# Kernel tuning notes

Measured on AMD Instinct MI355X. Metric: run time of the kernel, lower is better.

Reference implementation:

```python
import jax, jax.numpy as jnp
import numpy as np

B, S, D = 1, 2048, 1024
H, DH = 16, 64
FF_INNER = 4 * D          # 4096
FUSED = 2 * FF_INNER      # 8192
ROT_BASE = 1000.0


def _rope_tables(seq_len, dim_head):
    # rotarizer: inv_freq = (base ** (arange(0, dh, 2)/dh)) ** -1 ; cached in bfloat16
    inv_freq = 1.0 / (ROT_BASE ** (jnp.arange(0, dim_head, 2, dtype=jnp.float32) / dim_head))
    t = jnp.arange(seq_len, dtype=jnp.float32)
    freqs = jnp.outer(t, inv_freq)                     # [S, DH/2]
    cos = jnp.cos(freqs).astype(jnp.bfloat16)[None, :, None, :]  # [1,S,1,DH/2]
    sin = jnp.sin(freqs).astype(jnp.bfloat16)[None, :, None, :]
    return cos, sin


def _apply_rope(x, cos, sin):
    d = x.shape[-1] // 2
    x1, x2 = x[..., :d], x[..., d:]
    y1 = x1 * cos + x2 * sin
    y2 = -x1 * sin + x2 * cos
    return jnp.concatenate([y1, y2], axis=-1).astype(x.dtype)


def _l2norm(x):
    # F.normalize(p=2, dim=-1), eps=1e-12
    n = jnp.linalg.norm(x, axis=-1, keepdims=True)
    return x / jnp.maximum(n, 1e-12)


def setup_inputs() -> dict:
    key = jax.random.key(0)
    ks = jax.random.split(key, 12)
    std = 0.02
    inp = {
        "h_states": jax.random.normal(ks[0], (B, S, D), jnp.float32),
        "Wq": jax.random.normal(ks[1], (D, D), jnp.float32) * std,
        "Wk": jax.random.normal(ks[2], (D, D), jnp.float32) * std,
        "Wv": jax.random.normal(ks[3], (D, D), jnp.float32) * std,
        "Wqb": jax.random.normal(ks[4], (D, D), jnp.float32) * std,
        "Wkb": jax.random.normal(ks[5], (D, D), jnp.float32) * std,
        "Wo": jax.random.normal(ks[6], (D, D), jnp.float32) * std,
        "bo": jnp.zeros((D,), jnp.float32),
        "W1": jax.random.normal(ks[7], (D, FUSED), jnp.float32) * std,
        "b1": jnp.zeros((FUSED,), jnp.float32),
        "W2": jax.random.normal(ks[8], (FF_INNER, D), jnp.float32) * std,
        "b2": jnp.zeros((D,), jnp.float32),
        "learnedlambda": jnp.asarray(1.0, jnp.float32),
        # l2normscale init: log(S^2 - S) for training_seqlen S
        "l2normscale": jnp.asarray(np.log(float(S) ** 2 - float(S)), np.float32),
    }
    return inp


def reference(h_states, Wq, Wk, Wv, Wqb, Wkb, Wo, bo, W1, b1, W2, b2, learnedlambda, l2normscale):
    b, s, d = h_states.shape
    scale = DH ** -0.5

    # layerwisenorm: RMSNorm, no affine
    eps = jnp.finfo(h_states.dtype).eps
    x = h_states * jax.lax.rsqrt(jnp.mean(jnp.square(h_states), axis=-1, keepdims=True) + eps)

    # projections -> [B,S,H,DH]
    def proj(W):
        return (x @ W).reshape(b, s, H, DH)
    q, k, v = proj(Wq), proj(Wk), proj(Wv)
    qb, kb = proj(Wqb), proj(Wkb)

    cos, sin = _rope_tables(s, DH)
    # per-head qk-norm (l2norm) then rope; v untouched
    q = _apply_rope(_l2norm(q), cos, sin)
    k = _apply_rope(_l2norm(k), cos, sin)
    qb = _apply_rope(_l2norm(qb), cos, sin)
    kb = _apply_rope(_l2norm(kb), cos, sin)

    causal = jnp.tril(jnp.ones((s, s), bool))  # [S,S]

    # main attention: scale=1 (l2norm path), causal softmax, scaled by l2normscale
    scores = jnp.einsum("bqhd,bkhd->bhqk", q, k)
    scores = jnp.where(causal[None, None], scores, -jnp.inf)
    attn = jax.nn.softmax(scores, axis=-1)
    y = l2normscale * jnp.einsum("bhqk,bkhd->bhqd", attn, v)  # [B,H,S,DH]

    # bias attention: masked raw scores @ ones == causal row-sum, broadcast over DH
    sb = jnp.einsum("bqhd,bkhd->bhqk", qb, kb) * scale
    sb = jnp.where(causal[None, None], sb, 0.0)
    y = y + jnp.sum(sb, axis=-1, keepdims=True)  # broadcast over head dim

    y = y.transpose(0, 2, 1, 3).reshape(b, s, d)
    attn_out = y @ Wo + bo

    # fused SwiGLU: chunk -> (x_part, gate); silu(gate) * x_part
    u = x @ W1 + b1
    xp, gate = u[..., :FF_INNER], u[..., FF_INNER:]
    ff = (jax.nn.silu(gate) * xp) @ W2 + b2

    return h_states * learnedlambda + ff + attn_out
```

## Files before the change

### kernel.cpp

```cpp
#include <hip/hip_runtime.h>
#include <hip/hip_bf16.h>
#include <math.h>

typedef __bf16 bf16x8 __attribute__((ext_vector_type(8)));
typedef float  f32x4  __attribute__((ext_vector_type(4)));

#define GLD16(g, l) __builtin_amdgcn_global_load_lds(                      \
    (const __attribute__((address_space(1))) void*)(g),                    \
    (__attribute__((address_space(3))) void*)(l), 16, 0, 0)

#define SCHED_FENCE() __builtin_amdgcn_sched_barrier(0)


__device__ __forceinline__ void tconv_tile(const float* __restrict__ in,
                                           __bf16* __restrict__ out,
                                           int ldin, int ldout,
                                           int r0, int c0, int tid) {
  __shared__ float t[32][33];
  int tx = tid & 31, ty = tid >> 5;
  #pragma unroll
  for (int i = ty; i < 32; i += 8)
    t[i][tx] = in[(size_t)(r0 + i) * ldin + c0 + tx];
  __syncthreads();
  #pragma unroll
  for (int i = ty; i < 32; i += 8)
    out[(size_t)(c0 + i) * ldout + r0 + tx] = (__bf16)t[tx][i];
}

__global__ __launch_bounds__(256) void tconv_k(const float* __restrict__ in,
                                               __bf16* __restrict__ out,
                                               int ldin, int ldout) {
  tconv_tile(in, out, ldin, ldout, blockIdx.y * 32, blockIdx.x * 32, threadIdx.x);
}

__global__ __launch_bounds__(256) void tconvw1p_k(const float* __restrict__ W1,
                                                  __bf16* __restrict__ out) {
  int c0 = blockIdx.x * 32;
  int src_c0 = ((c0 >> 5) & 1) * 4096 + (c0 >> 6) * 32;
  __shared__ float t[32][33];
  int r0 = blockIdx.y * 32;
  int tid = threadIdx.x, tx = tid & 31, ty = tid >> 5;
  #pragma unroll
  for (int i = ty; i < 32; i += 8)
    t[i][tx] = W1[(size_t)(r0 + i) * 8192 + src_c0 + tx];
  __syncthreads();
  #pragma unroll
  for (int i = ty; i < 32; i += 8)
    out[(size_t)(c0 + i) * 1024 + r0 + tx] = (__bf16)t[tx][i];
}

__global__ __launch_bounds__(256) void tconv5_k(const float* __restrict__ w0,
    const float* __restrict__ w1, const float* __restrict__ w2,
    const float* __restrict__ w3, const float* __restrict__ w4,
    __bf16* __restrict__ out) {
  const float* src[5] = {w0, w1, w2, w3, w4};
  int z = blockIdx.z;
  tconv_tile(src[z], out + (size_t)z * 1048576, 1024, 1024,
             blockIdx.y * 32, blockIdx.x * 32, threadIdx.x);
}

__global__ __launch_bounds__(256) void tconvwow2_k(const float* __restrict__ Wo,
    const float* __restrict__ W2, __bf16* __restrict__ WoW2t) {
  int tid = threadIdx.x;
  if (blockIdx.z == 0) {
    if (blockIdx.y >= 32) return;
    __shared__ float t[32][33];
    int r0 = blockIdx.y * 32, c0 = blockIdx.x * 32;
    int tx = tid & 31, ty = tid >> 5;
    #pragma unroll
    for (int i = ty; i < 32; i += 8)
      t[i][tx] = Wo[(size_t)(r0 + i) * 1024 + c0 + tx];
    __syncthreads();
    #pragma unroll
    for (int i = ty; i < 32; i += 8)
      WoW2t[(size_t)(c0 + i) * 5120 + r0 + tx] = (__bf16)t[tx][i];
  } else {
    __shared__ float t[32][33];
    int r0 = blockIdx.y * 32, c0 = blockIdx.x * 32;
    int tx = tid & 31, ty = tid >> 5;
    #pragma unroll
    for (int i = ty; i < 32; i += 8)
      t[i][tx] = W2[(size_t)(r0 + i) * 1024 + c0 + tx];
    __syncthreads();
    #pragma unroll
    for (int i = ty; i < 32; i += 8)
      WoW2t[(size_t)(c0 + i) * 5120 + 1024 + r0 + tx] = (__bf16)t[tx][i];
  }
}

__global__ __launch_bounds__(256) void rmsnorm_k(const float* __restrict__ hs,
                                                 __bf16* __restrict__ x) {
  int row = blockIdx.x, tid = threadIdx.x;
  const float4 v = ((const float4*)(hs + (size_t)row * 1024))[tid];
  float ss = v.x * v.x + v.y * v.y + v.z * v.z + v.w * v.w;
  #pragma unroll
  for (int o = 32; o > 0; o >>= 1) ss += __shfl_xor(ss, o);
  __shared__ float ps[4];
  if ((tid & 63) == 0) ps[tid >> 6] = ss;
  __syncthreads();
  float tot = ps[0] + ps[1] + ps[2] + ps[3];
  float r = rsqrtf(tot * (1.0f / 1024.0f) + 1.1920929e-7f);
  __bf16* xr = x + (size_t)row * 1024 + tid * 4;
  xr[0] = (__bf16)(v.x * r); xr[1] = (__bf16)(v.y * r);
  xr[2] = (__bf16)(v.z * r); xr[3] = (__bf16)(v.w * r);
}

__global__ __launch_bounds__(256, 3) void gemm_bt_k(
    const __bf16* __restrict__ A, const __bf16* __restrict__ Bt,
    float* __restrict__ C, int N, int K) {
  __shared__ __bf16 sA[3][128 * 32];
  __shared__ __bf16 sB[3][128 * 32];
  const int tid = threadIdx.x;
  const int lane = tid & 63;
  const int quad = lane >> 4, l16 = lane & 15;
  const int wave = tid >> 6;
  const int waveM = wave >> 1, waveN = wave & 1;
  const int m0 = blockIdx.y * 128, n0 = blockIdx.x * 128;
  const int nk = K >> 5;
  const int rowS = tid >> 2;
  const int kg = ((tid & 3) ^ ((rowS >> 1) & 3)) * 8;
  const __bf16* gA0 = A + (size_t)(m0 + rowS) * K + kg;
  const __bf16* gA1 = gA0 + (size_t)64 * K;
  const __bf16* gB0 = Bt + (size_t)(n0 + rowS) * K + kg;
  const __bf16* gB1 = gB0 + (size_t)64 * K;
  const int lo0 = tid * 8, lo1 = 2048 + tid * 8;

  auto stage = [&](int t) {
    int s = t % 3;
    __bf16* dA = sA[s];
    __bf16* dB = sB[s];
    GLD16(gA0 + t * 32, dA + lo0);
    GLD16(gA1 + t * 32, dA + lo1);
    GLD16(gB0 + t * 32, dB + lo0);
    GLD16(gB1 + t * 32, dB + lo1);
  };
  stage(0); stage(1);

  f32x4 acc[4][4] = {};
  #pragma unroll 1
  for (int i = 0; i < nk; ++i) {
    if (i < nk - 1)
      asm volatile("s_waitcnt vmcnt(4)" ::: "memory");
    else
      asm volatile("s_waitcnt vmcnt(0)" ::: "memory");
    __builtin_amdgcn_s_barrier();
    SCHED_FENCE();
    int cs = i % 3;
    const __bf16* cA = sA[cs];
    const __bf16* cB = sB[cs];
    if (i + 2 < nk) stage(i + 2);
    SCHED_FENCE();
    bf16x8 af[4], bfv[4];
    #pragma unroll
    for (int mt = 0; mt < 4; ++mt) {
      int r = waveM * 64 + mt * 16 + l16;
      af[mt] = *(const bf16x8*)(cA + r * 32 + ((quad ^ ((r >> 1) & 3)) * 8));
    }
    #pragma unroll
    for (int nt = 0; nt < 4; ++nt) {
      int r = waveN * 64 + nt * 16 + l16;
      bfv[nt] = *(const bf16x8*)(cB + r * 32 + ((quad ^ ((r >> 1) & 3)) * 8));
    }
    __builtin_amdgcn_s_setprio(1);
    #pragma unroll
    for (int mt = 0; mt < 4; ++mt)
      #pragma unroll
      for (int nt = 0; nt < 4; ++nt)
        acc[mt][nt] = __builtin_amdgcn_mfma_f32_16x16x32_bf16(af[mt], bfv[nt], acc[mt][nt], 0, 0, 0);
    __builtin_amdgcn_s_setprio(0);
    SCHED_FENCE();
  }
  #pragma unroll
  for (int mt = 0; mt < 4; ++mt) {
    int row = m0 + waveM * 64 + mt * 16 + quad * 4;
    #pragma unroll
    for (int nt = 0; nt < 4; ++nt) {
      int col = n0 + waveN * 64 + nt * 16 + l16;
      #pragma unroll
      for (int r = 0; r < 4; ++r)
        C[(size_t)(row + r) * N + col] = acc[mt][nt][r];
    }
  }
}

__global__ __launch_bounds__(256, 3) void gemm_partk_k(
    const __bf16* __restrict__ A, const __bf16* __restrict__ Bt,
    float* __restrict__ P, int N, int K) {
  __shared__ __bf16 sA[3][128 * 32];
  __shared__ __bf16 sB[3][128 * 32];
  const int tid = threadIdx.x;
  const int lane = tid & 63;
  const int quad = lane >> 4, l16 = lane & 15;
  const int wave = tid >> 6;
  const int waveM = wave >> 1, waveN = wave & 1;
  const int m0 = blockIdx.y * 128, n0 = blockIdx.x * 128;
  const int kz = blockIdx.z, nz = gridDim.z;
  const int kper = K / nz, kbeg = kz * kper;
  const int nk = kper >> 5;
  const size_t MN = (size_t)gridDim.y * 128 * N;
  float* C = P + (size_t)kz * MN;
  const int rowS = tid >> 2;
  const int kg = ((tid & 3) ^ ((rowS >> 1) & 3)) * 8;
  const __bf16* gA0 = A + (size_t)(m0 + rowS) * K + kbeg + kg;
  const __bf16* gA1 = gA0 + (size_t)64 * K;
  const __bf16* gB0 = Bt + (size_t)(n0 + rowS) * K + kbeg + kg;
  const __bf16* gB1 = gB0 + (size_t)64 * K;
  const int lo0 = tid * 8, lo1 = 2048 + tid * 8;

  auto stage = [&](int t) {
    int s = t % 3;
    __bf16* dA = sA[s];
    __bf16* dB = sB[s];
    GLD16(gA0 + t * 32, dA + lo0);
    GLD16(gA1 + t * 32, dA + lo1);
    GLD16(gB0 + t * 32, dB + lo0);
    GLD16(gB1 + t * 32, dB + lo1);
  };
  stage(0); stage(1);

  f32x4 acc[4][4] = {};
  #pragma unroll 1
  for (int i = 0; i < nk; ++i) {
    if (i < nk - 1)
      asm volatile("s_waitcnt vmcnt(4)" ::: "memory");
    else
      asm volatile("s_waitcnt vmcnt(0)" ::: "memory");
    __builtin_amdgcn_s_barrier();
    SCHED_FENCE();
    int cs = i % 3;
    const __bf16* cA = sA[cs];
    const __bf16* cB = sB[cs];
    if (i + 2 < nk) stage(i + 2);
    SCHED_FENCE();
    bf16x8 af[4], bfv[4];
    #pragma unroll
    for (int mt = 0; mt < 4; ++mt) {
      int r = waveM * 64 + mt * 16 + l16;
      af[mt] = *(const bf16x8*)(cA + r * 32 + ((quad ^ ((r >> 1) & 3)) * 8));
    }
    #pragma unroll
    for (int nt = 0; nt < 4; ++nt) {
      int r = waveN * 64 + nt * 16 + l16;
      bfv[nt] = *(const bf16x8*)(cB + r * 32 + ((quad ^ ((r >> 1) & 3)) * 8));
    }
    __builtin_amdgcn_s_setprio(1);
    #pragma unroll
    for (int mt = 0; mt < 4; ++mt)
      #pragma unroll
      for (int nt = 0; nt < 4; ++nt)
        acc[mt][nt] = __builtin_amdgcn_mfma_f32_16x16x32_bf16(af[mt], bfv[nt], acc[mt][nt], 0, 0, 0);
    __builtin_amdgcn_s_setprio(0);
    SCHED_FENCE();
  }
  #pragma unroll
  for (int mt = 0; mt < 4; ++mt) {
    int row = m0 + waveM * 64 + mt * 16 + quad * 4;
    #pragma unroll
    for (int nt = 0; nt < 4; ++nt) {
      int col = n0 + waveN * 64 + nt * 16 + l16;
      #pragma unroll
      for (int r = 0; r < 4; ++r)
        C[(size_t)(row + r) * N + col] = acc[mt][nt][r];
    }
  }
}

__global__ __launch_bounds__(512, 2) void ffn1silu_k(
    const __bf16* __restrict__ A, const __bf16* __restrict__ W1t,
    const float* __restrict__ b1, __bf16* __restrict__ ffout) {
  __shared__ __bf16 sA[4][256 * 32];
  __shared__ __bf16 sB[4][256 * 32];
  const int tid = threadIdx.x, lane = tid & 63, w = tid >> 6;
  const int quad = lane >> 4, l16 = lane & 15;
  const int wm = w >> 2, wn = w & 3;
  const int m0 = blockIdx.y * 256;
  const int n0p = blockIdx.x * 256;
  const int K = 1024, NKT = 32;
  const int rowS = tid >> 2;
  const int kg = ((tid & 3) ^ ((rowS >> 1) & 3)) * 8;
  const __bf16* gA0 = A + (size_t)(m0 + rowS) * K + kg;
  const __bf16* gA1 = gA0 + (size_t)128 * K;
  const __bf16* gB0 = W1t + (size_t)(n0p + rowS) * K + kg;
  const __bf16* gB1 = gB0 + (size_t)128 * K;
  const int lo0 = tid * 8, lo1 = 4096 + tid * 8;

  f32x4 acc[8][4] = {};

  auto stageA = [&](int t) {
    __bf16* d = sA[t & 3];
    GLD16(gA0 + t * 32, d + lo0);
    GLD16(gA1 + t * 32, d + lo1);
  };
  auto stageB = [&](int t) {
    __bf16* d = sB[t & 3];
    GLD16(gB0 + t * 32, d + lo0);
    GLD16(gB1 + t * 32, d + lo1);
  };

  auto compute_half = [&](const __bf16* cA, const bf16x8* bfr, int half) {
    bf16x8 af[4];
    #pragma unroll
    for (int mt = 0; mt < 4; ++mt) {
      int r = wm * 128 + half * 64 + mt * 16 + l16;
      af[mt] = *(const bf16x8*)(cA + r * 32 + ((quad ^ ((r >> 1) & 3)) * 8));
    }
    __builtin_amdgcn_s_setprio(1);
    #pragma unroll
    for (int mt = 0; mt < 4; ++mt)
      #pragma unroll
      for (int nt = 0; nt < 4; ++nt)
        acc[half * 4 + mt][nt] = __builtin_amdgcn_mfma_f32_16x16x32_bf16(
            af[mt], bfr[nt], acc[half * 4 + mt][nt], 0, 0, 0);
    __builtin_amdgcn_s_setprio(0);
  };

  stageA(0); stageB(0);
  stageA(1); stageB(1);
  stageA(2); stageB(2);

  #pragma unroll 1
  for (int t = 0; t < NKT; ++t) {
    if (t < NKT - 2)
      asm volatile("s_waitcnt vmcnt(8)" ::: "memory");
    else if (t == NKT - 2)
      asm volatile("s_waitcnt vmcnt(4)" ::: "memory");
    else
      asm volatile("s_waitcnt vmcnt(0)" ::: "memory");
    __builtin_amdgcn_s_barrier();
    SCHED_FENCE();
    const __bf16* cA = sA[t & 3];
    const __bf16* cB = sB[t & 3];
    if (t + 3 < NKT) stageA(t + 3);
    SCHED_FENCE();
    bf16x8 bfr[4];
    #pragma unroll
    for (int nt = 0; nt < 4; ++nt) {
      int r = wn * 64 + nt * 16 + l16;
      bfr[nt] = *(const bf16x8*)(cB + r * 32 + ((quad ^ ((r >> 1) & 3)) * 8));
    }
    compute_half(cA, bfr, 0);
    SCHED_FENCE();
    if (t + 3 < NKT) stageB(t + 3);
    SCHED_FENCE();
    compute_half(cA, bfr, 1);
    SCHED_FENCE();
  }

  const int colbase = (blockIdx.x * 4 + wn) * 32;
  #pragma unroll
  for (int j = 0; j < 8; ++j) {
    int row = m0 + wm * 128 + (j >> 2) * 64 + (j & 3) * 16 + quad * 4;
    #pragma unroll
    for (int p = 0; p < 2; ++p) {
      int col = colbase + p * 16 + l16;
      float bxv = b1[col], bgv = b1[col + 4096];
      #pragma unroll
      for (int r = 0; r < 4; ++r) {
        float xp = acc[j][p][r] + bxv;
        float g  = acc[j][p + 2][r] + bgv;
        float val = xp * g / (1.f + __expf(-g));
        ffout[(size_t)(row + r) * 5120 + 1024 + col] = (__bf16)val;
      }
    }
  }
}

__global__ __launch_bounds__(256) void combine_k(
    const float* __restrict__ P, const float* __restrict__ b2,
    const float* __restrict__ bo, const float* __restrict__ hs,
    const float* __restrict__ plam, float* __restrict__ out) {
  const size_t MN = (size_t)2048 * 1024;
  size_t i = ((size_t)blockIdx.x * 256 + threadIdx.x) * 4;
  int col = (int)(i & 1023);
  float4 a0 = *(const float4*)(P + i);
  float4 a1 = *(const float4*)(P + MN + i);
  float4 a2 = *(const float4*)(P + 2 * MN + i);
  float4 a3 = *(const float4*)(P + 3 * MN + i);
  float4 h  = *(const float4*)(hs + i);
  float4 v2 = *(const float4*)(b2 + col);
  float4 vo = *(const float4*)(bo + col);
  float lam = plam[0];
  float4 o;
  o.x = (a0.x + a1.x) + (a2.x + a3.x) + v2.x + vo.x + lam * h.x;
  o.y = (a0.y + a1.y) + (a2.y + a3.y) + v2.y + vo.y + lam * h.y;
  o.z = (a0.z + a1.z) + (a2.z + a3.z) + v2.z + vo.z + lam * h.z;
  o.w = (a0.w + a1.w) + (a2.w + a3.w) + v2.w + vo.w + lam * h.w;
  *(float4*)(out + i) = o;
}

__global__ __launch_bounds__(256) void qkprep_k(const float* __restrict__ proj,
    __bf16* __restrict__ qo, __bf16* __restrict__ ko,
    float* __restrict__ qbo, float* __restrict__ kbo) {
  int gw = blockIdx.x * 4 + (threadIdx.x >> 6);
  int lane = threadIdx.x & 63;
  int s = gw >> 4, h = gw & 15;
  int j = lane & 31;
  float inv = exp2f(-0.31143076f * (float)j);
  float ang = (float)s * inv;
  float cb = (float)(__bf16)__cosf(ang);
  float sb = (float)(__bf16)__sinf(ang);
  size_t ibase = (size_t)s * 5120 + h * 64 + lane;
  size_t obase = (size_t)s * 1024 + h * 64 + lane;
  bool lo = lane < 32;

  auto proc = [&](const float* src) -> float {
    float xv = src[ibase];
    float ss = xv * xv;
    #pragma unroll
    for (int o = 32; o > 0; o >>= 1) ss += __shfl_xor(ss, o);
    float y = xv / fmaxf(sqrtf(ss), 1e-12f);
    float yp = __shfl_xor(y, 32);
    return lo ? (y * cb + yp * sb) : (y * cb - yp * sb);
  };
  qo[obase]  = (__bf16)proc(proj + 0);
  ko[obase]  = (__bf16)proc(proj + 1024);
  qbo[obase] = proc(proj + 3072);
  kbo[obase] = proc(proj + 4096);
}

__global__ __launch_bounds__(256) void kbsum_k(const float* __restrict__ kb,
                                               float* __restrict__ tsum,
                                               float* __restrict__ tsum8) {
  int t = blockIdx.x, h = blockIdx.y;
  int d = threadIdx.x & 63, w = threadIdx.x >> 6;
  size_t base = (size_t)h * 64 + d;
  float s = 0.f;
  #pragma unroll
  for (int r = 0; r < 8; ++r)
    s += kb[(size_t)(t * 32 + w * 8 + r) * 1024 + base];
  tsum8[(size_t)((t * 4 + w) * 16 + h) * 64 + d] = s;
  __shared__ float ps[4][64];
  ps[w][d] = s;
  __syncthreads();
  if (w == 0)
    tsum[(size_t)(t * 16 + h) * 64 + d] = (ps[0][d] + ps[1][d]) + (ps[2][d] + ps[3][d]);
}

__global__ __launch_bounds__(256) void sbrow2_k(const float* __restrict__ qb,
                                                const float* __restrict__ kb,
                                                const float* __restrict__ tsum,
                                                const float* __restrict__ tsum8,
                                                float* __restrict__ sb) {
  int t = blockIdx.x, h = blockIdx.y;
  int d = threadIdx.x & 63, g = threadIdx.x >> 6;
  size_t base = (size_t)h * 64 + d;
  float run = 0.f;
  for (int tp = 0; tp < t; ++tp) run += tsum[(size_t)(tp * 16 + h) * 64 + d];
  for (int w = 0; w < g; ++w) run += tsum8[(size_t)((t * 4 + w) * 16 + h) * 64 + d];
  int r0 = t * 32 + g * 8;
  for (int s0 = 0; s0 < 8; s0 += 4) {
    float p[4];
    #pragma unroll
    for (int u = 0; u < 4; ++u) {
      size_t off = (size_t)(r0 + s0 + u) * 1024 + base;
      run += kb[off];
      p[u] = qb[off] * run;
    }
    #pragma unroll
    for (int o = 32; o > 0; o >>= 1) {
      #pragma unroll
      for (int u = 0; u < 4; ++u) p[u] += __shfl_xor(p[u], o);
    }
    if (d == 0) {
      #pragma unroll
      for (int u = 0; u < 4; ++u) sb[(r0 + s0 + u) * 16 + h] = 0.125f * p[u];
    }
  }
}

__global__ __launch_bounds__(256) void attn_k(const __bf16* __restrict__ qg,
    const __bf16* __restrict__ kg, const __bf16* __restrict__ vtg,
    float* __restrict__ o_part, float* __restrict__ m_part,
    float* __restrict__ l_part) {
  __shared__ __bf16 sK[2][64 * 64];
  __shared__ __bf16 sVt[2][64 * 64];
  __shared__ __bf16 sP[4][16 * 64];
  const int pair = blockIdx.x, j4 = blockIdx.y, hh = blockIdx.z;
  const int tid = threadIdx.x, lane = tid & 63, w = tid >> 6;
  const int quad = lane >> 4, l16 = lane & 15;
  const int srow = tid >> 3;
  const int sg = (tid & 7) ^ (srow & 7);
  __bf16* sPw = sP[w];

  auto stage = [&](int kt) {
    int b = kt & 1;
    const __bf16* gK = kg + (size_t)(kt * 64 + srow) * 1024 + hh * 64 + sg * 8;
    const __bf16* gV = vtg + (size_t)(hh * 64 + srow) * 2048 + kt * 64 + sg * 8;
    GLD16(gK, sK[b] + tid * 8);
    GLD16(gK + (size_t)32 * 1024, sK[b] + tid * 8 + 2048);
    GLD16(gV, sVt[b] + tid * 8);
    GLD16(gV + (size_t)32 * 2048, sVt[b] + tid * 8 + 2048);
  };

  for (int phase = 0; phase < 2; ++phase) {
    const int qt = phase ? 31 - pair : pair;
    const int q0 = qt * 64;
    const int n = qt + 1;
    const int kb = (j4 * n) >> 2, ke = ((j4 + 1) * n) >> 2;
    bf16x8 qf[2];
    #pragma unroll
    for (int kk = 0; kk < 2; ++kk)
      qf[kk] = *(const bf16x8*)(qg + (size_t)(q0 + w * 16 + l16) * 1024 + hh * 64 + kk * 32 + quad * 8);
    f32x4 accO[4] = {};
    float m_[4], l_[4];
    #pragma unroll
    for (int r = 0; r < 4; ++r) { m_[r] = -INFINITY; l_[r] = 0.f; }

    __syncthreads();
    if (kb < ke) stage(kb);

    for (int kt = kb; kt < ke; ++kt) {
      __syncthreads();
      SCHED_FENCE();
      if (kt + 1 < ke) stage(kt + 1);
      SCHED_FENCE();
      const __bf16* cK = sK[kt & 1];
      const __bf16* cV = sVt[kt & 1];

      f32x4 s4[4];
      #pragma unroll
      for (int nt = 0; nt < 4; ++nt) {
        int r = nt * 16 + l16;
        bf16x8 b0 = *(const bf16x8*)(cK + r * 64 + ((quad ^ (r & 7)) * 8));
        bf16x8 b1 = *(const bf16x8*)(cK + r * 64 + (((4 + quad) ^ (r & 7)) * 8));
        f32x4 sa = {0.f, 0.f, 0.f, 0.f};
        sa = __builtin_amdgcn_mfma_f32_16x16x32_bf16(qf[0], b0, sa, 0, 0, 0);
        sa = __builtin_amdgcn_mfma_f32_16x16x32_bf16(qf[1], b1, sa, 0, 0, 0);
        s4[nt] = sa;
      }
      if (kt == qt) {
        #pragma unroll
        for (int nt = 0; nt < 4; ++nt)
          #pragma unroll
          for (int r = 0; r < 4; ++r)
            if (nt * 16 + l16 > w * 16 + quad * 4 + r) s4[nt][r] = -INFINITY;
      }
      float mx[4], al[4], rs[4];
      #pragma unroll
      for (int r = 0; r < 4; ++r)
        mx[r] = fmaxf(fmaxf(s4[0][r], s4[1][r]), fmaxf(s4[2][r], s4[3][r]));
      #pragma unroll
      for (int o = 1; o < 16; o <<= 1)
        #pragma unroll
        for (int r = 0; r < 4; ++r) mx[r] = fmaxf(mx[r], __shfl_xor(mx[r], o));
      #pragma unroll
      for (int r = 0; r < 4; ++r) {
        float mn = fmaxf(m_[r], mx[r]);
        al[r] = __expf(m_[r] - mn);
        m_[r] = mn;
      }
      float p[4][4];
      #pragma unroll
      for (int nt = 0; nt < 4; ++nt)
        #pragma unroll
        for (int r = 0; r < 4; ++r)
          p[nt][r] = __expf(s4[nt][r] - m_[r]);
      #pragma unroll
      for (int r = 0; r < 4; ++r)
        rs[r] = (p[0][r] + p[1][r]) + (p[2][r] + p[3][r]);
      #pragma unroll
      for (int o = 1; o < 16; o <<= 1)
        #pragma unroll
        for (int r = 0; r < 4; ++r) rs[r] += __shfl_xor(rs[r], o);
      #pragma unroll
      for (int r = 0; r < 4; ++r) l_[r] = l_[r] * al[r] + rs[r];
      #pragma unroll
      for (int nt = 0; nt < 4; ++nt)
        #pragma unroll
        for (int r = 0; r < 4; ++r) accO[nt][r] *= al[r];
      #pragma unroll
      for (int nt = 0; nt < 4; ++nt)
        #pragma unroll
        for (int r = 0; r < 4; ++r) {
          int row = quad * 4 + r, col = nt * 16 + l16;
          sPw[row * 64 + (col ^ ((row & 7) << 3))] = (__bf16)p[nt][r];
        }
      #pragma unroll
      for (int kk = 0; kk < 2; ++kk) {
        bf16x8 a = *(const bf16x8*)(sPw + l16 * 64 + (((kk * 4 + quad) ^ (l16 & 7)) * 8));
        #pragma unroll
        for (int nt = 0; nt < 4; ++nt) {
          int vr = nt * 16 + l16;
          bf16x8 bv = *(const bf16x8*)(cV + vr * 64 + (((kk * 4 + quad) ^ (vr & 7)) * 8));
          accO[nt] = __builtin_amdgcn_mfma_f32_16x16x32_bf16(a, bv, accO[nt], 0, 0, 0);
        }
      }
    }
    #pragma unroll
    for (int r = 0; r < 4; ++r) {
      int grow = q0 + w * 16 + quad * 4 + r;
      if (l16 == 0) {
        m_part[((size_t)j4 * 2048 + grow) * 16 + hh] = m_[r];
        l_part[((size_t)j4 * 2048 + grow) * 16 + hh] = l_[r];
      }
      #pragma unroll
      for (int nt = 0; nt < 4; ++nt)
        o_part[((size_t)j4 * 2048 + grow) * 1024 + hh * 64 + nt * 16 + l16] = accO[nt][r];
    }
  }
}

__global__ __launch_bounds__(256) void attnmerge_k(const float* __restrict__ o_part,
    const float* __restrict__ m_part, const float* __restrict__ l_part,
    const float* __restrict__ sbr, const float* __restrict__ pl2s,
    __bf16* __restrict__ yo) {
  int idx = blockIdx.x * 256 + threadIdx.x;
  int s = idx >> 8, rem = idx & 255;
  int h = rem >> 4, dg = (rem & 15) * 4;
  float m[4], l[4];
  #pragma unroll
  for (int j = 0; j < 4; ++j) {
    m[j] = m_part[((size_t)j * 2048 + s) * 16 + h];
    l[j] = l_part[((size_t)j * 2048 + s) * 16 + h];
  }
  float M = fmaxf(fmaxf(m[0], m[1]), fmaxf(m[2], m[3]));
  float den = 0.f;
  float4 acc = {0.f, 0.f, 0.f, 0.f};
  #pragma unroll
  for (int j = 0; j < 4; ++j) {
    float e = __expf(m[j] - M);
    den += l[j] * e;
    float4 o = *(const float4*)(o_part + ((size_t)j * 2048 + s) * 1024 + h * 64 + dg);
    acc.x += e * o.x; acc.y += e * o.y; acc.z += e * o.z; acc.w += e * o.w;
  }
  float sc = pl2s[0] / den;
  float add = sbr[s * 16 + h];
  __bf16* yp = yo + (size_t)s * 5120 + h * 64 + dg;
  yp[0] = (__bf16)(sc * acc.x + add);
  yp[1] = (__bf16)(sc * acc.y + add);
  yp[2] = (__bf16)(sc * acc.z + add);
  yp[3] = (__bf16)(sc * acc.w + add);
}

extern "C" void kernel_launch(void* const* d_in, const int* in_sizes, int n_in,
                              void* d_out, int out_size, void* d_ws, size_t ws_size,
                              hipStream_t stream) {
  (void)in_sizes; (void)n_in; (void)out_size; (void)ws_size;
  const float* hs   = (const float*)d_in[0];
  const float* Wq   = (const float*)d_in[1];
  const float* Wk   = (const float*)d_in[2];
  const float* Wv   = (const float*)d_in[3];
  const float* Wqb  = (const float*)d_in[4];
  const float* Wkb  = (const float*)d_in[5];
  const float* Wo   = (const float*)d_in[6];
  const float* bo   = (const float*)d_in[7];
  const float* W1   = (const float*)d_in[8];
  const float* b1   = (const float*)d_in[9];
  const float* W2   = (const float*)d_in[10];
  const float* b2   = (const float*)d_in[11];
  const float* plam = (const float*)d_in[12];
  const float* pl2s = (const float*)d_in[13];
  float* out = (float*)d_out;
  char* ws = (char*)d_ws;

  size_t off = 0;
  auto alloc = [&](size_t bytes) { char* p = ws + off; off += (bytes + 255) & ~(size_t)255; return p; };
  __bf16* Wt5    = (__bf16*)alloc((size_t)5 * 1024 * 1024 * 2);
  __bf16* WoW2t  = (__bf16*)alloc((size_t)1024 * 5120 * 2);
  __bf16* W1t    = (__bf16*)alloc((size_t)8192 * 1024 * 2);
  __bf16* xbf    = (__bf16*)alloc((size_t)2048 * 1024 * 2);
  __bf16* concat = (__bf16*)alloc((size_t)2048 * 5120 * 2);
  float*  proj  = (float*)alloc((size_t)2048 * 5120 * 4);
  float*  qbf32 = (float*)alloc((size_t)2048 * 1024 * 4);
  float*  kbf32 = (float*)alloc((size_t)2048 * 1024 * 4);
  __bf16* qbf   = (__bf16*)alloc((size_t)2048 * 1024 * 2);
  __bf16* kbf   = (__bf16*)alloc((size_t)2048 * 1024 * 2);
  float*  o_part = proj;
  float*  m_part = qbf32;
  float*  l_part = qbf32 + (size_t)4 * 2048 * 16;
  float*  gpart  = proj;
  __bf16* vtbf  = (__bf16*)alloc((size_t)1024 * 2048 * 2);
  float*  sbrow = (float*)alloc((size_t)2048 * 16 * 4);
  float*  tsum  = (float*)alloc((size_t)64 * 16 * 64 * 4);
  float*  tsum8 = (float*)alloc((size_t)256 * 16 * 64 * 4);

  tconv5_k<<<dim3(32, 32, 5), 256, 0, stream>>>(Wq, Wk, Wv, Wqb, Wkb, Wt5);
  tconvwow2_k<<<dim3(32, 128, 2), 256, 0, stream>>>(Wo, W2, WoW2t);
  tconvw1p_k<<<dim3(256, 32), 256, 0, stream>>>(W1, W1t);

  rmsnorm_k<<<2048, 256, 0, stream>>>(hs, xbf);
  gemm_bt_k<<<dim3(40, 16), 256, 0, stream>>>(xbf, Wt5, proj, 5120, 1024);
  qkprep_k<<<8192, 256, 0, stream>>>(proj, qbf, kbf, qbf32, kbf32);
  tconv_k<<<dim3(32, 64), 256, 0, stream>>>(proj + 2048, vtbf, 5120, 2048);
  kbsum_k<<<dim3(64, 16), 256, 0, stream>>>(kbf32, tsum, tsum8);
  sbrow2_k<<<dim3(64, 16), 256, 0, stream>>>(qbf32, kbf32, tsum, tsum8, sbrow);
  attn_k<<<dim3(16, 4, 16), 256, 0, stream>>>(qbf, kbf, vtbf, o_part, m_part, l_part);
  attnmerge_k<<<2048, 256, 0, stream>>>(o_part, m_part, l_part, sbrow, pl2s, concat);
  ffn1silu_k<<<dim3(32, 8), 512, 0, stream>>>(xbf, W1t, b1, concat);
  gemm_partk_k<<<dim3(8, 16, 4), 256, 0, stream>>>(concat, WoW2t, gpart, 1024, 5120);
  combine_k<<<2048, 256, 0, stream>>>(gpart, b2, bo, hs, plam, out);
}
```

Measured before the change: 361.2 us.

## Fuse qk l2norm+RoPE into QKV GEMM epilogue and merge weight repack launches

Moves the per-head L2 normalization and rotary embedding into the QKV projection GEMM's epilogue. Each wave's 64-column tile is exactly one head, so the norm is a 16-lane shuffle reduction, and q/k/qb/kb are written directly in their final formats. V is written to a compact buffer. This removes the separate qkprep kernel and the write and read-back of the full fp32 projection. The three weight transpose/convert kernels are also merged into one flat-grid repack kernel to cut launch overhead. The cost is extra epilogue math and more registers in the GEMM.

```diff
diff --git a/kernel.cpp b/kernel.cpp
--- a/kernel.cpp
+++ b/kernel.cpp
@@ -12,12 +12,56 @@
 #define SCHED_FENCE() __builtin_amdgcn_sched_barrier(0)
 
 
-__device__ __forceinline__ void tconv_tile(const float* __restrict__ in,
-                                           __bf16* __restrict__ out,
-                                           int ldin, int ldout,
-                                           int r0, int c0, int tid) {
+__global__ __launch_bounds__(256) void repack_k(
+    const float* __restrict__ Wq, const float* __restrict__ Wk,
+    const float* __restrict__ Wv, const float* __restrict__ Wqb,
+    const float* __restrict__ Wkb, const float* __restrict__ Wo,
+    const float* __restrict__ W2, const float* __restrict__ W1,
+    __bf16* __restrict__ Wt5, __bf16* __restrict__ WoW2t,
+    __bf16* __restrict__ W1t) {
+  int t = blockIdx.x;
+  const float* in; __bf16* outp;
+  int ldin, ldout, r0, c0, cin0, oofs;
+  if (t < 5120) {
+    int w = t >> 10, rem = t & 1023;
+    const float* src[5] = {Wq, Wk, Wv, Wqb, Wkb};
+    in = src[w]; ldin = 1024;
+    r0 = (rem >> 5) << 5; c0 = (rem & 31) << 5; cin0 = c0;
+    outp = Wt5 + (size_t)w * 1048576; ldout = 1024; oofs = 0;
+  } else if (t < 6144) {
+    int rem = t - 5120;
+    in = Wo; ldin = 1024;
+    r0 = (rem >> 5) << 5; c0 = (rem & 31) << 5; cin0 = c0;
+    outp = WoW2t; ldout = 5120; oofs = 0;
+  } else if (t < 10240) {
+    int rem = t - 6144;
+    in = W2; ldin = 1024;
+    r0 = (rem >> 5) << 5; c0 = (rem & 31) << 5; cin0 = c0;
+    outp = WoW2t; ldout = 5120; oofs = 1024;
+  } else {
+    int rem = t - 10240;
+    in = W1; ldin = 8192;
+    c0 = (rem & 255) << 5; r0 = (rem >> 8) << 5;
+    cin0 = ((c0 >> 5) & 1) * 4096 + (c0 >> 6) * 32;
+    outp = W1t; ldout = 1024; oofs = 0;
+  }
+  __shared__ float sh[32][33];
+  int tid = threadIdx.x, tx = tid & 31, ty = tid >> 5;
+  #pragma unroll
+  for (int i = ty; i < 32; i += 8)
+    sh[i][tx] = in[(size_t)(r0 + i) * ldin + cin0 + tx];
+  __syncthreads();
+  #pragma unroll
+  for (int i = ty; i < 32; i += 8)
+    outp[(size_t)(c0 + i) * ldout + oofs + r0 + tx] = (__bf16)sh[tx][i];
+}
+
+__global__ __launch_bounds__(256) void tconv_k(const float* __restrict__ in,
+                                               __bf16* __restrict__ out,
+                                               int ldin, int ldout) {
   __shared__ float t[32][33];
-  int tx = tid & 31, ty = tid >> 5;
+  int r0 = blockIdx.y * 32, c0 = blockIdx.x * 32;
+  int tid = threadIdx.x, tx = tid & 31, ty = tid >> 5;
   #pragma unroll
   for (int i = ty; i < 32; i += 8)
     t[i][tx] = in[(size_t)(r0 + i) * ldin + c0 + tx];
@@ -25,67 +69,6 @@
   #pragma unroll
   for (int i = ty; i < 32; i += 8)
     out[(size_t)(c0 + i) * ldout + r0 + tx] = (__bf16)t[tx][i];
-}
-
-__global__ __launch_bounds__(256) void tconv_k(const float* __restrict__ in,
-                                               __bf16* __restrict__ out,
-                                               int ldin, int ldout) {
-  tconv_tile(in, out, ldin, ldout, blockIdx.y * 32, blockIdx.x * 32, threadIdx.x);
-}
-
-__global__ __launch_bounds__(256) void tconvw1p_k(const float* __restrict__ W1,
-                                                  __bf16* __restrict__ out) {
-  int c0 = blockIdx.x * 32;
-  int src_c0 = ((c0 >> 5) & 1) * 4096 + (c0 >> 6) * 32;
-  __shared__ float t[32][33];
-  int r0 = blockIdx.y * 32;
-  int tid = threadIdx.x, tx = tid & 31, ty = tid >> 5;
-  #pragma unroll
-  for (int i = ty; i < 32; i += 8)
-    t[i][tx] = W1[(size_t)(r0 + i) * 8192 + src_c0 + tx];
-  __syncthreads();
-  #pragma unroll
-  for (int i = ty; i < 32; i += 8)
-    out[(size_t)(c0 + i) * 1024 + r0 + tx] = (__bf16)t[tx][i];
-}
-
-__global__ __launch_bounds__(256) void tconv5_k(const float* __restrict__ w0,
-    const float* __restrict__ w1, const float* __restrict__ w2,
-    const float* __restrict__ w3, const float* __restrict__ w4,
-    __bf16* __restrict__ out) {
-  const float* src[5] = {w0, w1, w2, w3, w4};
-  int z = blockIdx.z;
-  tconv_tile(src[z], out + (size_t)z * 1048576, 1024, 1024,
-             blockIdx.y * 32, blockIdx.x * 32, threadIdx.x);
-}
-
-__global__ __launch_bounds__(256) void tconvwow2_k(const float* __restrict__ Wo,
-    const float* __restrict__ W2, __bf16* __restrict__ WoW2t) {
-  int tid = threadIdx.x;
-  if (blockIdx.z == 0) {
-    if (blockIdx.y >= 32) return;
-    __shared__ float t[32][33];
-    int r0 = blockIdx.y * 32, c0 = blockIdx.x * 32;
-    int tx = tid & 31, ty = tid >> 5;
-    #pragma unroll
-    for (int i = ty; i < 32; i += 8)
-      t[i][tx] = Wo[(size_t)(r0 + i) * 1024 + c0 + tx];
-    __syncthreads();
-    #pragma unroll
-    for (int i = ty; i < 32; i += 8)
-      WoW2t[(size_t)(c0 + i) * 5120 + r0 + tx] = (__bf16)t[tx][i];
-  } else {
-    __shared__ float t[32][33];
-    int r0 = blockIdx.y * 32, c0 = blockIdx.x * 32;
-    int tx = tid & 31, ty = tid >> 5;
-    #pragma unroll
-    for (int i = ty; i < 32; i += 8)
-      t[i][tx] = W2[(size_t)(r0 + i) * 1024 + c0 + tx];
-    __syncthreads();
-    #pragma unroll
-    for (int i = ty; i < 32; i += 8)
-      WoW2t[(size_t)(c0 + i) * 5120 + 1024 + r0 + tx] = (__bf16)t[tx][i];
-  }
 }
 
 __global__ __launch_bounds__(256) void rmsnorm_k(const float* __restrict__ hs,
@@ -105,9 +88,12 @@
   xr[2] = (__bf16)(v.z * r); xr[3] = (__bf16)(v.w * r);
 }
 
-__global__ __launch_bounds__(256, 3) void gemm_bt_k(
+__global__ __launch_bounds__(256, 3) void gemm_qkv_k(
     const __bf16* __restrict__ A, const __bf16* __restrict__ Bt,
-    float* __restrict__ C, int N, int K) {
+    __bf16* __restrict__ qbf, __bf16* __restrict__ kbf,
+    float* __restrict__ qb32, float* __restrict__ kb32,
+    float* __restrict__ vproj) {
+  const int K = 1024;
   __shared__ __bf16 sA[3][128 * 32];
   __shared__ __bf16 sB[3][128 * 32];
   const int tid = threadIdx.x;
@@ -170,15 +156,61 @@
     __builtin_amdgcn_s_setprio(0);
     SCHED_FENCE();
   }
-  #pragma unroll
-  for (int mt = 0; mt < 4; ++mt) {
-    int row = m0 + waveM * 64 + mt * 16 + quad * 4;
-    #pragma unroll
-    for (int nt = 0; nt < 4; ++nt) {
-      int col = n0 + waveN * 64 + nt * 16 + l16;
-      #pragma unroll
-      for (int r = 0; r < 4; ++r)
-        C[(size_t)(row + r) * N + col] = acc[mt][nt][r];
+
+  const int wid = n0 >> 10;
+  const int cw0 = (n0 & 1023) + waveN * 64;
+  if (wid == 2) {
+    #pragma unroll
+    for (int mt = 0; mt < 4; ++mt) {
+      int row = m0 + waveM * 64 + mt * 16 + quad * 4;
+      #pragma unroll
+      for (int nt = 0; nt < 4; ++nt) {
+        int col = cw0 + nt * 16 + l16;
+        #pragma unroll
+        for (int r = 0; r < 4; ++r)
+          vproj[(size_t)(row + r) * 1024 + col] = acc[mt][nt][r];
+      }
+    }
+  } else {
+    const float inv0 = exp2f(-0.31143076f * (float)l16);
+    const float inv1 = exp2f(-0.31143076f * (float)(16 + l16));
+    #pragma unroll
+    for (int mt = 0; mt < 4; ++mt) {
+      #pragma unroll
+      for (int r = 0; r < 4; ++r) {
+        int srow = m0 + waveM * 64 + mt * 16 + quad * 4 + r;
+        float a0 = acc[mt][0][r], a1 = acc[mt][1][r];
+        float a2 = acc[mt][2][r], a3 = acc[mt][3][r];
+        float ss = a0 * a0 + a1 * a1 + a2 * a2 + a3 * a3;
+        ss += __shfl_xor(ss, 1); ss += __shfl_xor(ss, 2);
+        ss += __shfl_xor(ss, 4); ss += __shfl_xor(ss, 8);
+        float yn = 1.0f / fmaxf(sqrtf(ss), 1e-12f);
+        float ang0 = (float)srow * inv0;
+        float cb0 = (float)(__bf16)__cosf(ang0);
+        float sb0 = (float)(__bf16)__sinf(ang0);
+        float ang1 = (float)srow * inv1;
+        float cb1 = (float)(__bf16)__cosf(ang1);
+        float sb1 = (float)(__bf16)__sinf(ang1);
+        float y0 = a0 * yn, y1 = a1 * yn, y2 = a2 * yn, y3 = a3 * yn;
+        float o0 =  y0 * cb0 + y2 * sb0;
+        float o1 =  y1 * cb1 + y3 * sb1;
+        float o2 = -y0 * sb0 + y2 * cb0;
+        float o3 = -y1 * sb1 + y3 * cb1;
+        size_t base = (size_t)srow * 1024 + cw0 + l16;
+        if (wid == 0) {
+          qbf[base]      = (__bf16)o0; qbf[base + 16] = (__bf16)o1;
+          qbf[base + 32] = (__bf16)o2; qbf[base + 48] = (__bf16)o3;
+        } else if (wid == 1) {
+          kbf[base]      = (__bf16)o0; kbf[base + 16] = (__bf16)o1;
+          kbf[base + 32] = (__bf16)o2; kbf[base + 48] = (__bf16)o3;
+        } else if (wid == 3) {
+          qb32[base]      = o0; qb32[base + 16] = o1;
+          qb32[base + 32] = o2; qb32[base + 48] = o3;
+        } else {
+          kb32[base]      = o0; kb32[base + 16] = o1;
+          kb32[base + 32] = o2; kb32[base + 48] = o3;
+        }
+      }
     }
   }
 }
@@ -388,36 +420,6 @@
   *(float4*)(out + i) = o;
 }
 
-__global__ __launch_bounds__(256) void qkprep_k(const float* __restrict__ proj,
-    __bf16* __restrict__ qo, __bf16* __restrict__ ko,
-    float* __restrict__ qbo, float* __restrict__ kbo) {
-  int gw = blockIdx.x * 4 + (threadIdx.x >> 6);
-  int lane = threadIdx.x & 63;
-  int s = gw >> 4, h = gw & 15;
-  int j = lane & 31;
-  float inv = exp2f(-0.31143076f * (float)j);
-  float ang = (float)s * inv;
-  float cb = (float)(__bf16)__cosf(ang);
-  float sb = (float)(__bf16)__sinf(ang);
-  size_t ibase = (size_t)s * 5120 + h * 64 + lane;
-  size_t obase = (size_t)s * 1024 + h * 64 + lane;
-  bool lo = lane < 32;
-
-  auto proc = [&](const float* src) -> float {
-    float xv = src[ibase];
-    float ss = xv * xv;
-    #pragma unroll
-    for (int o = 32; o > 0; o >>= 1) ss += __shfl_xor(ss, o);
-    float y = xv / fmaxf(sqrtf(ss), 1e-12f);
-    float yp = __shfl_xor(y, 32);
-    return lo ? (y * cb + yp * sb) : (y * cb - yp * sb);
-  };
-  qo[obase]  = (__bf16)proc(proj + 0);
-  ko[obase]  = (__bf16)proc(proj + 1024);
-  qbo[obase] = proc(proj + 3072);
-  kbo[obase] = proc(proj + 4096);
-}
-
 __global__ __launch_bounds__(256) void kbsum_k(const float* __restrict__ kb,
                                                float* __restrict__ tsum,
                                                float* __restrict__ tsum8) {
@@ -665,6 +667,7 @@
   float*  kbf32 = (float*)alloc((size_t)2048 * 1024 * 4);
   __bf16* qbf   = (__bf16*)alloc((size_t)2048 * 1024 * 2);
   __bf16* kbf   = (__bf16*)alloc((size_t)2048 * 1024 * 2);
+  float*  vproj  = proj;
   float*  o_part = proj;
   float*  m_part = qbf32;
   float*  l_part = qbf32 + (size_t)4 * 2048 * 16;
@@ -674,14 +677,13 @@
   float*  tsum  = (float*)alloc((size_t)64 * 16 * 64 * 4);
   float*  tsum8 = (float*)alloc((size_t)256 * 16 * 64 * 4);
 
-  tconv5_k<<<dim3(32, 32, 5), 256, 0, stream>>>(Wq, Wk, Wv, Wqb, Wkb, Wt5);
-  tconvwow2_k<<<dim3(32, 128, 2), 256, 0, stream>>>(Wo, W2, WoW2t);
-  tconvw1p_k<<<dim3(256, 32), 256, 0, stream>>>(W1, W1t);
+  repack_k<<<18432, 256, 0, stream>>>(Wq, Wk, Wv, Wqb, Wkb, Wo, W2, W1,
+                                      Wt5, WoW2t, W1t);
 
   rmsnorm_k<<<2048, 256, 0, stream>>>(hs, xbf);
-  gemm_bt_k<<<dim3(40, 16), 256, 0, stream>>>(xbf, Wt5, proj, 5120, 1024);
-  qkprep_k<<<8192, 256, 0, stream>>>(proj, qbf, kbf, qbf32, kbf32);
-  tconv_k<<<dim3(32, 64), 256, 0, stream>>>(proj + 2048, vtbf, 5120, 2048);
+  gemm_qkv_k<<<dim3(40, 16), 256, 0, stream>>>(xbf, Wt5, qbf, kbf,
+                                               qbf32, kbf32, vproj);
+  tconv_k<<<dim3(32, 64), 256, 0, stream>>>(vproj, vtbf, 1024, 2048);
   kbsum_k<<<dim3(64, 16), 256, 0, stream>>>(kbf32, tsum, tsum8);
   sbrow2_k<<<dim3(64, 16), 256, 0, stream>>>(qbf32, kbf32, tsum, tsum8, sbrow);
   attn_k<<<dim3(16, 4, 16), 256, 0, stream>>>(qbf, kbf, vtbf, o_part, m_part, l_part);
```

Result: faster. 344.0 us (-4.8%).
